# Kernel optimization log

Hardware: AMD Instinct MI355X
Metric: run time of the kernel (lower is better)

Reference implementation:

```python
import jax, jax.numpy as jnp
import numpy as np

D_MODEL = 256
D_STATE = 256          # n_state == embedding_dim in this module
D_INNER = 2 * D_MODEL  # mamba expand=2
DT_RANK = D_MODEL // 16
D_CONV = 4
N_BLOCKS = 2
BATCH, SEQLEN = 2, 512


def setup_inputs() -> dict:
    key = jax.random.key(0)
    ks = jax.random.split(key, 10)

    def rn(k, shape, s=0.02):
        return (jax.random.normal(k, shape) * s).astype(jnp.float32)

    # S4D-real style A init: A_log = log(1..d_state), tiled per channel
    A_log = jnp.tile(
        jnp.log(jnp.arange(1, D_STATE + 1, dtype=jnp.float32))[None, None, :],
        (N_BLOCKS, D_INNER, 1),
    )
    return {
        "x": jax.random.normal(ks[0], (BATCH, SEQLEN, D_MODEL), dtype=jnp.float32),
        "in_proj_w": rn(ks[1], (N_BLOCKS, 2 * D_INNER, D_MODEL)),
        "conv_w": rn(ks[2], (N_BLOCKS, D_INNER, D_CONV), 0.3),
        "conv_b": jnp.zeros((N_BLOCKS, D_INNER), jnp.float32),
        "x_proj_w": rn(ks[3], (N_BLOCKS, DT_RANK + 2 * D_STATE, D_INNER)),
        "dt_proj_w": rn(ks[4], (N_BLOCKS, D_INNER, DT_RANK), 0.1),
        # softplus^{-1}(0.01): dt starts around 0.01 as in mamba init
        "dt_proj_b": jnp.full((N_BLOCKS, D_INNER), float(np.log(np.expm1(0.01))), jnp.float32),
        "A_log": A_log,
        "D": jnp.ones((N_BLOCKS, D_INNER), jnp.float32),
        "out_proj_w": rn(ks[5], (N_BLOCKS, D_MODEL, D_INNER)),
        "ffn_w1": rn(ks[6], (N_BLOCKS, 4 * D_MODEL, D_MODEL)),
        "ffn_b1": jnp.zeros((N_BLOCKS, 4 * D_MODEL), jnp.float32),
        "ffn_w2": rn(ks[7], (N_BLOCKS, D_MODEL, 4 * D_MODEL)),
        "ffn_b2": jnp.zeros((N_BLOCKS, D_MODEL), jnp.float32),
    }


def _mamba(x, in_w, cw, cb, xpw, dtw, dtb, A_log, Dp, ow):
    Bb, Ls, _ = x.shape
    xz = jnp.einsum('bld,ed->ble', x, in_w)            # (B,L,2*d_inner)
    xc, z = jnp.split(xz, 2, axis=-1)
    # causal depthwise conv1d over time (kernel D_CONV, left pad D_CONV-1)
    xp = jnp.pad(xc, ((0, 0), (D_CONV - 1, 0), (0, 0)))
    xconv = sum(xp[:, k:k + Ls, :] * cw[:, k] for k in range(D_CONV)) + cb
    xconv = jax.nn.silu(xconv)                          # (B,L,d_inner)
    x_dbl = jnp.einsum('bld,ed->ble', xconv, xpw)       # (B,L,dt_rank+2*d_state)
    dt = x_dbl[..., :DT_RANK]
    Bm = x_dbl[..., DT_RANK:DT_RANK + D_STATE]
    Cm = x_dbl[..., DT_RANK + D_STATE:]
    dt = jax.nn.softplus(jnp.einsum('blr,dr->bld', dt, dtw) + dtb)  # (B,L,d_inner)
    A = -jnp.exp(A_log)                                 # (d_inner,d_state)

    def step(h, inp):
        dt_t, B_t, C_t, x_t = inp                       # (B,di),(B,ds),(B,ds),(B,di)
        h = jnp.exp(dt_t[..., None] * A) * h + (dt_t * x_t)[..., None] * B_t[:, None, :]
        return h, jnp.einsum('bds,bs->bd', h, C_t)

    h0 = jnp.zeros((Bb, D_INNER, D_STATE), dtype=x.dtype)
    _, ys = jax.lax.scan(
        step, h0,
        (dt.swapaxes(0, 1), Bm.swapaxes(0, 1), Cm.swapaxes(0, 1), xconv.swapaxes(0, 1)),
    )
    y = ys.swapaxes(0, 1) + xconv * Dp
    y = y * jax.nn.silu(z)
    return jnp.einsum('bld,ed->ble', y, ow)


def reference(x, in_proj_w, conv_w, conv_b, x_proj_w, dt_proj_w, dt_proj_b,
              A_log, D, out_proj_w, ffn_w1, ffn_b1, ffn_w2, ffn_b2):
    # VanillaMambaBlock.forward: x = ffn(mamba(x))  (norms/residual unused in source)
    for i in range(N_BLOCKS):
        h = _mamba(x, in_proj_w[i], conv_w[i], conv_b[i], x_proj_w[i],
                   dt_proj_w[i], dt_proj_b[i], A_log[i], D[i], out_proj_w[i])
        h = jax.nn.gelu(jnp.einsum('bld,fd->blf', h, ffn_w1[i]) + ffn_b1[i], approximate=False)
        x = jnp.einsum('blf,ef->ble', h, ffn_w2[i]) + ffn_b2[i]
    return x
```

## Files before the change

kernel.cpp:

```cpp
#include <hip/hip_runtime.h>
#include <math.h>

#define BATCHN 2
#define SEQLEN 512
#define DMODEL 256
#define DSTATE 256
#define DINNER 512
#define DTRANK 16
#define MROWS (BATCHN * SEQLEN)

typedef float f32x4 __attribute__((ext_vector_type(4)));
typedef __bf16 bf16x8 __attribute__((ext_vector_type(8)));

__device__ __forceinline__ float gelu_exact(float v) {
    return 0.5f * v * (1.0f + erff(v * 0.70710678118654752440f));
}
__device__ __forceinline__ float softplus_f(float v) {
    return fmaxf(v, 0.0f) + log1pf(__expf(-fabsf(v)));
}
__device__ __forceinline__ float silu_f(float v) {
    return v / (1.0f + __expf(-v));
}

#define DPP_ADD(X, CTRL)                                                              \
    {                                                                                 \
        int dpp_t_ = __builtin_amdgcn_update_dpp(                                     \
            0, __builtin_bit_cast(int, (X)), (CTRL), 0xf, 0xf, true);                 \
        (X) += __builtin_bit_cast(float, dpp_t_);                                     \
    }
#define DPP_REDUCE32(X)                                                               \
    DPP_ADD(X, 0x111) DPP_ADD(X, 0x112) DPP_ADD(X, 0x114) DPP_ADD(X, 0x118)          \
    DPP_ADD(X, 0x142)

__device__ __forceinline__ void split8(float4 u, float4 v, bf16x8& hi, bf16x8& lo) {
#define SP8(idx, val) { __bf16 h_ = (__bf16)(val); hi[idx] = h_; lo[idx] = (__bf16)((val) - (float)h_); }
    SP8(0, u.x) SP8(1, u.y) SP8(2, u.z) SP8(3, u.w)
    SP8(4, v.x) SP8(5, v.y) SP8(6, v.z) SP8(7, v.w)
#undef SP8
}

template <int NF, int EPI>
__global__ __launch_bounds__(256) void gemm_mfma_kernel(
    const float* __restrict__ A, int lda,
    const float* __restrict__ W,
    const float* __restrict__ bias,
    float* __restrict__ C, int ldc,
    int N, int K)
{
    const int tid = threadIdx.x;
    const int wv = tid >> 6;
    const int lane = tid & 63;
    const int l15 = lane & 15;
    const int kgrp = lane >> 4;
    const int m0 = blockIdx.y * 64 + wv * 16;
    const int n0 = blockIdx.x * (16 * NF);

    const float* ap = A + (size_t)(m0 + l15) * lda + kgrp * 8;
    const float* bp[NF];
#pragma unroll
    for (int nf = 0; nf < NF; ++nf) {
        int col = n0 + nf * 16 + l15;
        if (col >= N) col = N - 1;
        bp[nf] = W + (size_t)col * K + kgrp * 8;
    }

    f32x4 acc[NF];
#pragma unroll
    for (int nf = 0; nf < NF; ++nf) acc[nf] = (f32x4){0.f, 0.f, 0.f, 0.f};

    float4 ar0 = *(const float4*)ap, ar1 = *(const float4*)(ap + 4);
    float4 br0[NF], br1[NF];
#pragma unroll
    for (int nf = 0; nf < NF; ++nf) {
        br0[nf] = *(const float4*)bp[nf];
        br1[nf] = *(const float4*)(bp[nf] + 4);
    }

    for (int k0 = 0; k0 < K; k0 += 32) {
        const int adv = (k0 + 32 < K) ? 32 : 0;
        ap += adv;
        float4 an0 = *(const float4*)ap, an1 = *(const float4*)(ap + 4);
        float4 bn0[NF], bn1[NF];
#pragma unroll
        for (int nf = 0; nf < NF; ++nf) {
            bp[nf] += adv;
            bn0[nf] = *(const float4*)bp[nf];
            bn1[nf] = *(const float4*)(bp[nf] + 4);
        }
        bf16x8 ahi, alo;
        split8(ar0, ar1, ahi, alo);
#pragma unroll
        for (int nf = 0; nf < NF; ++nf) {
            bf16x8 bhi, blo;
            split8(br0[nf], br1[nf], bhi, blo);
            acc[nf] = __builtin_amdgcn_mfma_f32_16x16x32_bf16(ahi, bhi, acc[nf], 0, 0, 0);
            acc[nf] = __builtin_amdgcn_mfma_f32_16x16x32_bf16(ahi, blo, acc[nf], 0, 0, 0);
            acc[nf] = __builtin_amdgcn_mfma_f32_16x16x32_bf16(alo, bhi, acc[nf], 0, 0, 0);
        }
        ar0 = an0; ar1 = an1;
#pragma unroll
        for (int nf = 0; nf < NF; ++nf) { br0[nf] = bn0[nf]; br1[nf] = bn1[nf]; }
    }

#pragma unroll
    for (int nf = 0; nf < NF; ++nf) {
        const int col = n0 + nf * 16 + l15;
        const bool cok = (col < N);
        float bv = 0.f;
        if (EPI >= 1 && cok) bv = bias[col];
#pragma unroll
        for (int j = 0; j < 4; ++j) {
            const int row = m0 + kgrp * 4 + j;
            float v = acc[nf][j];
            if (EPI >= 1) v += bv;
            if (EPI == 2) v = gelu_exact(v);
            if (cok) C[(size_t)row * ldc + col] = v;
        }
    }
}

template <int EPI>
__global__ __launch_bounds__(128) void gemm_kernel(
    const float* __restrict__ A, int lda,
    const float* __restrict__ W,
    const float* __restrict__ bias,
    float* __restrict__ C, int ldc,
    int M, int N, int K)
{
    __shared__ float As[32 * 32];
    __shared__ float Ws[32 * 32];
    const int tid = threadIdx.x;
    const int tx = tid & 15, ty = tid >> 4;
    const int m0 = blockIdx.y * 32, n0 = blockIdx.x * 32;
    const int lrow = tid >> 2;
    const int lk = (tid & 3) << 3;

    float acc[4][2] = {};

    for (int k0 = 0; k0 < K; k0 += 32) {
        const float* arow = A + (size_t)(m0 + lrow) * lda + k0 + lk;
        float4 a0 = *(const float4*)(arow);
        float4 a1 = *(const float4*)(arow + 4);
        int wrow = n0 + lrow;
        if (wrow >= N) wrow = N - 1;
        const float* wp = W + (size_t)wrow * K + k0 + lk;
        float4 w0 = {0,0,0,0}, w1 = {0,0,0,0};
        if (k0 + lk + 3 < K) w0 = *(const float4*)(wp);
        if (k0 + lk + 7 < K) w1 = *(const float4*)(wp + 4);
        __syncthreads();
        As[(lk + 0) * 32 + lrow] = a0.x;
        As[(lk + 1) * 32 + lrow] = a0.y;
        As[(lk + 2) * 32 + lrow] = a0.z;
        As[(lk + 3) * 32 + lrow] = a0.w;
        As[(lk + 4) * 32 + lrow] = a1.x;
        As[(lk + 5) * 32 + lrow] = a1.y;
        As[(lk + 6) * 32 + lrow] = a1.z;
        As[(lk + 7) * 32 + lrow] = a1.w;
        Ws[(lk + 0) * 32 + lrow] = w0.x;
        Ws[(lk + 1) * 32 + lrow] = w0.y;
        Ws[(lk + 2) * 32 + lrow] = w0.z;
        Ws[(lk + 3) * 32 + lrow] = w0.w;
        Ws[(lk + 4) * 32 + lrow] = w1.x;
        Ws[(lk + 5) * 32 + lrow] = w1.y;
        Ws[(lk + 6) * 32 + lrow] = w1.z;
        Ws[(lk + 7) * 32 + lrow] = w1.w;
        __syncthreads();
#pragma unroll
        for (int k = 0; k < 32; ++k) {
            float4 av = *(const float4*)(As + k * 32 + (ty << 2));
            float2 wv = *(const float2*)(Ws + k * 32 + (tx << 1));
            float ar[4] = {av.x, av.y, av.z, av.w};
            float wr[2] = {wv.x, wv.y};
#pragma unroll
            for (int i = 0; i < 4; ++i)
#pragma unroll
                for (int j = 0; j < 2; ++j)
                    acc[i][j] = fmaf(ar[i], wr[j], acc[i][j]);
        }
    }

#pragma unroll
    for (int i = 0; i < 4; ++i) {
        const int row = m0 + (ty << 2) + i;
#pragma unroll
        for (int j = 0; j < 2; ++j) {
            const int col = n0 + (tx << 1) + j;
            if (col < N) {
                float v = acc[i][j];
                if (EPI >= 1) v += bias[col];
                if (EPI == 2) v = gelu_exact(v);
                if (EPI == 3) v = softplus_f(v);
                C[(size_t)row * ldc + col] = v;
            }
        }
    }
}

__global__ __launch_bounds__(256) void conv_silu_kernel(
    const float* __restrict__ xz, const float* __restrict__ cw,
    const float* __restrict__ cb, float* __restrict__ xconv)
{
    int idx = blockIdx.x * blockDim.x + threadIdx.x;
    if (idx >= MROWS * DINNER) return;
    int d = idx & (DINNER - 1);
    int bl = idx >> 9;
    int l = bl & (SEQLEN - 1);
    int b = bl >> 9;
    float s = cb[d];
#pragma unroll
    for (int k = 0; k < 4; ++k) {
        int ls = l + k - 3;
        if (ls >= 0)
            s += xz[((size_t)(b * SEQLEN + ls)) * 1024 + d] * cw[d * 4 + k];
    }
    xconv[idx] = silu_f(s);
}

#define SCAN_STEP_A(DT, XV, ZV, B0, B1, C0, C1)                                      \
    {                                                                                \
        const float rho = __expf(-(DT));                                             \
        const float a0 = __expf(Afirst * (DT));                                      \
        const float val = (DT) * (XV);                                               \
        sumdt += (DT);                                                               \
        const float rho2 = rho * rho, rho4 = rho2 * rho2;                            \
        float a = a0;                                                                \
        h[0] = fmaf(a, h[0], val * (B0).x); float acA = h[0] * (C0).x; a *= rho;     \
        h[1] = fmaf(a, h[1], val * (B0).y); float acB = h[1] * (C0).y; a *= rho;     \
        h[2] = fmaf(a, h[2], val * (B0).z); acA = fmaf(h[2], (C0).z, acA); a *= rho; \
        h[3] = fmaf(a, h[3], val * (B0).w); acB = fmaf(h[3], (C0).w, acB);           \
        a = a0 * rho4;                                                               \
        h[4] = fmaf(a, h[4], val * (B1).x); acA = fmaf(h[4], (C1).x, acA); a *= rho; \
        h[5] = fmaf(a, h[5], val * (B1).y); acB = fmaf(h[5], (C1).y, acB); a *= rho; \
        h[6] = fmaf(a, h[6], val * (B1).z); acA = fmaf(h[6], (C1).z, acA); a *= rho; \
        h[7] = fmaf(a, h[7], val * (B1).w); acB = fmaf(h[7], (C1).w, acB);           \
        float acc = acA + acB;                                                       \
        DPP_REDUCE32(acc)                                                            \
        if (t == 31) y[o1 - 1024] = (acc + (XV) * Dd) * silu_f(ZV);                  \
    }

__global__ __launch_bounds__(256, 6) void scan_passA_kernel(
    const float* __restrict__ dtv, const float* __restrict__ xconv,
    const float* __restrict__ xdbl, const float* __restrict__ xz,
    const float* __restrict__ Dp,
    float* __restrict__ y, float* __restrict__ hend, float* __restrict__ sumdtb,
    int NC, int LC)
{
    const int c = blockIdx.x;
    const int bdo = blockIdx.y;
    const int b = bdo >> 6;
    const int tid = threadIdx.x;
    const int t = tid & 31;
    const int d = ((bdo & 63) << 3) + (tid >> 5);

    const float Afirst = -(float)(8 * t + 1);
    const float Dd = Dp[d];

    float h[8];
#pragma unroll
    for (int k = 0; k < 8; ++k) h[k] = 0.f;
    float sumdt = 0.f;

    const int bl0 = b * SEQLEN + c * LC;
    const float* xB = xdbl + 16;
    const float* xC = xdbl + 272;
    unsigned o1 = (unsigned)(bl0 * 512 + d);
    unsigned o2 = (unsigned)(bl0 * 1024 + 512 + d);
    unsigned o3 = (unsigned)(bl0 * 528 + t * 8);

    float dt0 = dtv[o1], xv0 = xconv[o1], zv0 = xz[o2];
    float4 B00 = *(const float4*)(xB + o3), B01 = *(const float4*)(xB + o3 + 4);
    float4 C00 = *(const float4*)(xC + o3), C01 = *(const float4*)(xC + o3 + 4);
    o1 += 512; o2 += 1024; o3 += 528;

    for (int il = 0; il < LC; il += 2) {
        float dt1 = dtv[o1], xv1 = xconv[o1], zv1 = xz[o2];
        float4 B10 = *(const float4*)(xB + o3), B11 = *(const float4*)(xB + o3 + 4);
        float4 C10 = *(const float4*)(xC + o3), C11 = *(const float4*)(xC + o3 + 4);
        o1 += 512; o2 += 1024; o3 += 528;
        SCAN_STEP_A(dt0, xv0, zv0, B00, B01, C00, C01);
        dt0 = dtv[o1]; xv0 = xconv[o1]; zv0 = xz[o2];
        B00 = *(const float4*)(xB + o3); B01 = *(const float4*)(xB + o3 + 4);
        C00 = *(const float4*)(xC + o3); C01 = *(const float4*)(xC + o3 + 4);
        o1 += 512; o2 += 1024; o3 += 528;
        SCAN_STEP_A(dt1, xv1, zv1, B10, B11, C10, C11);
    }

    const size_t sb = ((size_t)(b * 512 + d) * NC + c) * 256 + t * 8;
    *(float4*)(hend + sb)     = make_float4(h[0], h[1], h[2], h[3]);
    *(float4*)(hend + sb + 4) = make_float4(h[4], h[5], h[6], h[7]);
    if (t == 0) sumdtb[(size_t)(b * 512 + d) * NC + c] = sumdt;
}

__global__ __launch_bounds__(64) void scan_passB_kernel(
    float* __restrict__ hend, const float* __restrict__ sumdtb, int NC)
{
    const int bd = blockIdx.x;
    const int lane = threadIdx.x;
    const float As0 = -(float)(4 * lane + 1);
    const float As1 = As0 - 1.f, As2 = As0 - 2.f, As3 = As0 - 3.f;
    float4 hin = {0.f, 0.f, 0.f, 0.f};
    for (int c = 0; c < NC; ++c) {
        const float sdt = sumdtb[(size_t)bd * NC + c];
        const size_t sidx = ((size_t)bd * NC + c) * DSTATE + (lane << 2);
        float4 he = *(const float4*)(hend + sidx);
        float4 p;
        p.x = __expf(As0 * sdt);
        p.y = __expf(As1 * sdt);
        p.z = __expf(As2 * sdt);
        p.w = __expf(As3 * sdt);
        *(float4*)(hend + sidx) = hin;
        float4 nh;
        nh.x = fmaf(p.x, hin.x, he.x);
        nh.y = fmaf(p.y, hin.y, he.y);
        nh.z = fmaf(p.z, hin.z, he.z);
        nh.w = fmaf(p.w, hin.w, he.w);
        hin = nh;
    }
}

#define SCAN_STEP_C(DT, ZV, C0, C1)                                                  \
    {                                                                                \
        const float rho = __expf(-(DT));                                             \
        const float a0 = __expf(Afirst * (DT));                                      \
        const float rho2 = rho * rho, rho4 = rho2 * rho2;                            \
        float a = a0;                                                                \
        carry[0] *= a; float acA = carry[0] * (C0).x; a *= rho;                      \
        carry[1] *= a; float acB = carry[1] * (C0).y; a *= rho;                      \
        carry[2] *= a; acA = fmaf(carry[2], (C0).z, acA); a *= rho;                  \
        carry[3] *= a; acB = fmaf(carry[3], (C0).w, acB);                            \
        a = a0 * rho4;                                                               \
        carry[4] *= a; acA = fmaf(carry[4], (C1).x, acA); a *= rho;                  \
        carry[5] *= a; acB = fmaf(carry[5], (C1).y, acB); a *= rho;                  \
        carry[6] *= a; acA = fmaf(carry[6], (C1).z, acA); a *= rho;                  \
        carry[7] *= a; acB = fmaf(carry[7], (C1).w, acB);                            \
        float acc = acA + acB;                                                       \
        DPP_REDUCE32(acc)                                                            \
        if (t == 31) y[o1 - 1024] += acc * silu_f(ZV);                               \
    }

__global__ __launch_bounds__(256, 8) void scan_passC_kernel(
    const float* __restrict__ dtv, const float* __restrict__ xdbl,
    const float* __restrict__ xz, const float* __restrict__ hend,
    float* __restrict__ y, int NC, int LC)
{
    const int c = blockIdx.x + 1;
    const int bdo = blockIdx.y;
    const int b = bdo >> 6;
    const int tid = threadIdx.x;
    const int t = tid & 31;
    const int d = ((bdo & 63) << 3) + (tid >> 5);

    const float Afirst = -(float)(8 * t + 1);

    float carry[8];
    const size_t sb = ((size_t)(b * 512 + d) * NC + c) * 256 + t * 8;
    {
        float4 c0 = *(const float4*)(hend + sb);
        float4 c1 = *(const float4*)(hend + sb + 4);
        carry[0] = c0.x; carry[1] = c0.y; carry[2] = c0.z; carry[3] = c0.w;
        carry[4] = c1.x; carry[5] = c1.y; carry[6] = c1.z; carry[7] = c1.w;
    }

    const int bl0 = b * SEQLEN + c * LC;
    const float* xC = xdbl + 272;
    unsigned o1 = (unsigned)(bl0 * 512 + d);
    unsigned o2 = (unsigned)(bl0 * 1024 + 512 + d);
    unsigned o3 = (unsigned)(bl0 * 528 + t * 8);

    float dt0 = dtv[o1], zv0 = xz[o2];
    float4 C00 = *(const float4*)(xC + o3), C01 = *(const float4*)(xC + o3 + 4);
    o1 += 512; o2 += 1024; o3 += 528;

    for (int il = 0; il < LC; il += 2) {
        float dt1 = dtv[o1], zv1 = xz[o2];
        float4 C10 = *(const float4*)(xC + o3), C11 = *(const float4*)(xC + o3 + 4);
        o1 += 512; o2 += 1024; o3 += 528;
        SCAN_STEP_C(dt0, zv0, C00, C01);
        dt0 = dtv[o1]; zv0 = xz[o2];
        C00 = *(const float4*)(xC + o3); C01 = *(const float4*)(xC + o3 + 4);
        o1 += 512; o2 += 1024; o3 += 528;
        SCAN_STEP_C(dt1, zv1, C10, C11);
    }
}

extern "C" void kernel_launch(void* const* d_in, const int* in_sizes, int n_in,
                              void* d_out, int out_size, void* d_ws, size_t ws_size,
                              hipStream_t stream) {
    const float* x     = (const float*)d_in[0];
    const float* in_w  = (const float*)d_in[1];
    const float* cw    = (const float*)d_in[2];
    const float* cb    = (const float*)d_in[3];
    const float* xpw   = (const float*)d_in[4];
    const float* dtw   = (const float*)d_in[5];
    const float* dtb   = (const float*)d_in[6];
    const float* Dp    = (const float*)d_in[8];
    const float* ow    = (const float*)d_in[9];
    const float* w1    = (const float*)d_in[10];
    const float* b1    = (const float*)d_in[11];
    const float* w2    = (const float*)d_in[12];
    const float* b2    = (const float*)d_in[13];

    float* ws = (float*)d_ws;
    float* xzb   = ws;
    float* xcv   = xzb + 1024 * 1024;
    float* xdbl  = xcv + 1024 * 512;
    float* dtv   = xdbl + 1024 * 528;
    float* yb    = dtv + 1024 * 512;
    float* hendb = yb + 1024 * 512;
    const size_t baseFloats = 1024*1024 + 1024*512 + 1024*528 + 1024*512 + 1024*512;
    int NC = 16;
    while (NC > 1 && (baseFloats + (size_t)NC * 1024 * 256 + (size_t)NC * 1024) * 4ull > ws_size) NC >>= 1;
    const int LC = SEQLEN / NC;
    float* sumdtb = hendb + (size_t)NC * 1024 * 256;

    float* mo    = xcv;
    float* h1b   = xzb;
    float* x1    = xdbl;

    const float* xin = x;
    for (int i = 0; i < 2; ++i) {
        const float* inw_i = in_w + (size_t)i * 1024 * 256;
        const float* cw_i  = cw  + (size_t)i * 512 * 4;
        const float* cb_i  = cb  + (size_t)i * 512;
        const float* xpw_i = xpw + (size_t)i * 528 * 512;
        const float* dtw_i = dtw + (size_t)i * 512 * 16;
        const float* dtb_i = dtb + (size_t)i * 512;
        const float* Dp_i  = Dp  + (size_t)i * 512;
        const float* ow_i  = ow  + (size_t)i * 256 * 512;
        const float* w1_i  = w1  + (size_t)i * 1024 * 256;
        const float* b1_i  = b1  + (size_t)i * 1024;
        const float* w2_i  = w2  + (size_t)i * 256 * 1024;
        const float* b2_i  = b2  + (size_t)i * 256;

        gemm_mfma_kernel<2, 0><<<dim3(32, 16), 256, 0, stream>>>(xin, DMODEL, inw_i, nullptr, xzb, 1024, 1024, 256);
        conv_silu_kernel<<<(MROWS * DINNER + 255) / 256, 256, 0, stream>>>(xzb, cw_i, cb_i, xcv);
        gemm_mfma_kernel<2, 0><<<dim3(17, 16), 256, 0, stream>>>(xcv, DINNER, xpw_i, nullptr, xdbl, 528, 528, 512);
        gemm_kernel<3><<<dim3(16, 32), 128, 0, stream>>>(xdbl, 528, dtw_i, dtb_i, dtv, 512, MROWS, 512, 16);
        scan_passA_kernel<<<dim3(NC, 128), 256, 0, stream>>>(dtv, xcv, xdbl, xzb, Dp_i, yb, hendb, sumdtb, NC, LC);
        if (NC > 1) {
            scan_passB_kernel<<<MROWS, 64, 0, stream>>>(hendb, sumdtb, NC);
            scan_passC_kernel<<<dim3(NC - 1, 128), 256, 0, stream>>>(dtv, xdbl, xzb, hendb, yb, NC, LC);
        }
        gemm_mfma_kernel<1, 0><<<dim3(16, 16), 256, 0, stream>>>(yb, DINNER, ow_i, nullptr, mo, 256, 256, 512);
        gemm_mfma_kernel<2, 2><<<dim3(32, 16), 256, 0, stream>>>(mo, 256, w1_i, b1_i, h1b, 1024, 1024, 256);
        float* outp = (i == 1) ? (float*)d_out : x1;
        gemm_mfma_kernel<1, 1><<<dim3(16, 16), 256, 0, stream>>>(h1b, 1024, w2_i, b2_i, outp, 256, 256, 1024);
        xin = x1;
    }
}
```

Measured before the change: 356.9 us.

## Stage scan B/C and per-step scalars through double-buffered swizzled LDS

Scan passes A and C now load B/C rows and the dt/x/z scalars cooperatively into double-buffered shared memory, four timesteps at a time, instead of each wave loading them redundantly from global memory. A XOR swizzle on LDS addresses is meant to avoid bank conflicts on the float4 reads. The goal is to cut duplicated global and L2 traffic across the 8 channel-waves in a block. In exchange it adds a block-wide barrier every four steps, extra LDS use, and lowers pass A's occupancy hint from 6 to 5. It also assumes LC is a multiple of 4.

Result: faster. 335.2 us (-6.1%).

```diff
diff --git a/kernel.cpp b/kernel.cpp
--- a/kernel.cpp
+++ b/kernel.cpp
@@ -20,6 +20,9 @@
 }
 __device__ __forceinline__ float silu_f(float v) {
     return v / (1.0f + __expf(-v));
+}
+__device__ __forceinline__ unsigned swzw(unsigned w) {
+    return w ^ (((w >> 5) & 7u) << 2);
 }
 
 #define DPP_ADD(X, CTRL)                                                              \
@@ -216,73 +219,107 @@
     xconv[idx] = silu_f(s);
 }
 
-#define SCAN_STEP_A(DT, XV, ZV, B0, B1, C0, C1)                                      \
-    {                                                                                \
-        const float rho = __expf(-(DT));                                             \
-        const float a0 = __expf(Afirst * (DT));                                      \
-        const float val = (DT) * (XV);                                               \
-        sumdt += (DT);                                                               \
-        const float rho2 = rho * rho, rho4 = rho2 * rho2;                            \
-        float a = a0;                                                                \
-        h[0] = fmaf(a, h[0], val * (B0).x); float acA = h[0] * (C0).x; a *= rho;     \
-        h[1] = fmaf(a, h[1], val * (B0).y); float acB = h[1] * (C0).y; a *= rho;     \
-        h[2] = fmaf(a, h[2], val * (B0).z); acA = fmaf(h[2], (C0).z, acA); a *= rho; \
-        h[3] = fmaf(a, h[3], val * (B0).w); acB = fmaf(h[3], (C0).w, acB);           \
-        a = a0 * rho4;                                                               \
-        h[4] = fmaf(a, h[4], val * (B1).x); acA = fmaf(h[4], (C1).x, acA); a *= rho; \
-        h[5] = fmaf(a, h[5], val * (B1).y); acB = fmaf(h[5], (C1).y, acB); a *= rho; \
-        h[6] = fmaf(a, h[6], val * (B1).z); acA = fmaf(h[6], (C1).z, acA); a *= rho; \
-        h[7] = fmaf(a, h[7], val * (B1).w); acB = fmaf(h[7], (C1).w, acB);           \
-        float acc = acA + acB;                                                       \
-        DPP_REDUCE32(acc)                                                            \
-        if (t == 31) y[o1 - 1024] = (acc + (XV) * Dd) * silu_f(ZV);                  \
-    }
-
-__global__ __launch_bounds__(256, 6) void scan_passA_kernel(
+__global__ __launch_bounds__(256, 5) void scan_passA_kernel(
     const float* __restrict__ dtv, const float* __restrict__ xconv,
     const float* __restrict__ xdbl, const float* __restrict__ xz,
     const float* __restrict__ Dp,
     float* __restrict__ y, float* __restrict__ hend, float* __restrict__ sumdtb,
     int NC, int LC)
 {
+    __shared__ float bc[2][4][512];
+    __shared__ float ssc[2][3][4][8];
+
     const int c = blockIdx.x;
     const int bdo = blockIdx.y;
     const int b = bdo >> 6;
+    const int d0 = (bdo & 63) << 3;
     const int tid = threadIdx.x;
     const int t = tid & 31;
-    const int d = ((bdo & 63) << 3) + (tid >> 5);
+    const int hw = tid >> 5;
+    const int d = d0 + hw;
 
     const float Afirst = -(float)(8 * t + 1);
     const float Dd = Dp[d];
+    const int bl0 = b * SEQLEN + c * LC;
+
+    const int si = tid >> 7;
+    const int sF = tid & 127;
+    const unsigned wdst = swzw(4u * sF);
+    const int sarr = tid >> 5;
+    const int sri = (tid & 31) >> 3, sdd = tid & 7;
+    const float* pBC0 = xdbl + (size_t)(bl0 + si) * 528 + 16 + 4 * sF;
+    const float* pBC1 = pBC0 + 2 * 528;
+    const float* sbase;
+    unsigned sstep;
+    if (sarr == 0)      { sbase = dtv   + (size_t)(bl0 + sri) * 512 + d0 + sdd;        sstep = 2048; }
+    else if (sarr == 1) { sbase = xconv + (size_t)(bl0 + sri) * 512 + d0 + sdd;        sstep = 2048; }
+    else                { sbase = xz    + (size_t)(bl0 + sri) * 1024 + 512 + d0 + sdd; sstep = 4096; }
+
+    const unsigned sw = ((unsigned)(t >> 2)) << 2;
+    const unsigned wb0 = (8u * t) ^ sw;
+    const unsigned wb1 = (8u * t + 4u) ^ sw;
+    const unsigned wc0 = (256u + 8u * t) ^ sw;
+    const unsigned wc1 = (256u + 8u * t + 4u) ^ sw;
 
     float h[8];
 #pragma unroll
     for (int k = 0; k < 8; ++k) h[k] = 0.f;
     float sumdt = 0.f;
 
-    const int bl0 = b * SEQLEN + c * LC;
-    const float* xB = xdbl + 16;
-    const float* xC = xdbl + 272;
-    unsigned o1 = (unsigned)(bl0 * 512 + d);
-    unsigned o2 = (unsigned)(bl0 * 1024 + 512 + d);
-    unsigned o3 = (unsigned)(bl0 * 528 + t * 8);
-
-    float dt0 = dtv[o1], xv0 = xconv[o1], zv0 = xz[o2];
-    float4 B00 = *(const float4*)(xB + o3), B01 = *(const float4*)(xB + o3 + 4);
-    float4 C00 = *(const float4*)(xC + o3), C01 = *(const float4*)(xC + o3 + 4);
-    o1 += 512; o2 += 1024; o3 += 528;
-
-    for (int il = 0; il < LC; il += 2) {
-        float dt1 = dtv[o1], xv1 = xconv[o1], zv1 = xz[o2];
-        float4 B10 = *(const float4*)(xB + o3), B11 = *(const float4*)(xB + o3 + 4);
-        float4 C10 = *(const float4*)(xC + o3), C11 = *(const float4*)(xC + o3 + 4);
-        o1 += 512; o2 += 1024; o3 += 528;
-        SCAN_STEP_A(dt0, xv0, zv0, B00, B01, C00, C01);
-        dt0 = dtv[o1]; xv0 = xconv[o1]; zv0 = xz[o2];
-        B00 = *(const float4*)(xB + o3); B01 = *(const float4*)(xB + o3 + 4);
-        C00 = *(const float4*)(xC + o3); C01 = *(const float4*)(xC + o3 + 4);
-        o1 += 512; o2 += 1024; o3 += 528;
-        SCAN_STEP_A(dt1, xv1, zv1, B10, B11, C10, C11);
+    float4 rBC0 = *(const float4*)pBC0;
+    float4 rBC1 = *(const float4*)pBC1;
+    float rS = (sarr < 3) ? *sbase : 0.f;
+    *(float4*)&bc[0][si][wdst] = rBC0;
+    *(float4*)&bc[0][2 + si][wdst] = rBC1;
+    if (sarr < 3) ssc[0][sarr][sri][sdd] = rS;
+    __syncthreads();
+
+    const int G = LC >> 2;
+    unsigned ybase = (unsigned)(bl0 * 512 + d);
+    for (int g = 0; g < G; ++g) {
+        const int buf = g & 1;
+        if (g + 1 < G) {
+            rBC0 = *(const float4*)(pBC0 + (unsigned)(g + 1) * 2112u);
+            rBC1 = *(const float4*)(pBC1 + (unsigned)(g + 1) * 2112u);
+            if (sarr < 3) rS = sbase[(unsigned)(g + 1) * sstep];
+        }
+#pragma unroll
+        for (int i = 0; i < 4; ++i) {
+            const float dt = ssc[buf][0][i][hw];
+            const float xv = ssc[buf][1][i][hw];
+            const float zv = ssc[buf][2][i][hw];
+            const float* brow = &bc[buf][i][0];
+            float4 B0 = *(const float4*)(brow + wb0);
+            float4 B1 = *(const float4*)(brow + wb1);
+            float4 C0 = *(const float4*)(brow + wc0);
+            float4 C1 = *(const float4*)(brow + wc1);
+            const float rho = __expf(-dt);
+            const float a0 = __expf(Afirst * dt);
+            const float val = dt * xv;
+            sumdt += dt;
+            const float rho2 = rho * rho, rho4 = rho2 * rho2;
+            float a = a0;
+            h[0] = fmaf(a, h[0], val * B0.x); float acA = h[0] * C0.x; a *= rho;
+            h[1] = fmaf(a, h[1], val * B0.y); float acB = h[1] * C0.y; a *= rho;
+            h[2] = fmaf(a, h[2], val * B0.z); acA = fmaf(h[2], C0.z, acA); a *= rho;
+            h[3] = fmaf(a, h[3], val * B0.w); acB = fmaf(h[3], C0.w, acB);
+            a = a0 * rho4;
+            h[4] = fmaf(a, h[4], val * B1.x); acA = fmaf(h[4], C1.x, acA); a *= rho;
+            h[5] = fmaf(a, h[5], val * B1.y); acB = fmaf(h[5], C1.y, acB); a *= rho;
+            h[6] = fmaf(a, h[6], val * B1.z); acA = fmaf(h[6], C1.z, acA); a *= rho;
+            h[7] = fmaf(a, h[7], val * B1.w); acB = fmaf(h[7], C1.w, acB);
+            float acc = acA + acB;
+            DPP_REDUCE32(acc)
+            if (t == 31) y[ybase + i * 512] = (acc + xv * Dd) * silu_f(zv);
+        }
+        ybase += 2048;
+        if (g + 1 < G) {
+            const int nbuf = buf ^ 1;
+            *(float4*)&bc[nbuf][si][wdst] = rBC0;
+            *(float4*)&bc[nbuf][2 + si][wdst] = rBC1;
+            if (sarr < 3) ssc[nbuf][sarr][sri][sdd] = rS;
+        }
+        __syncthreads();
     }
 
     const size_t sb = ((size_t)(b * 512 + d) * NC + c) * 256 + t * 8;
@@ -318,39 +355,40 @@
     }
 }
 
-#define SCAN_STEP_C(DT, ZV, C0, C1)                                                  \
-    {                                                                                \
-        const float rho = __expf(-(DT));                                             \
-        const float a0 = __expf(Afirst * (DT));                                      \
-        const float rho2 = rho * rho, rho4 = rho2 * rho2;                            \
-        float a = a0;                                                                \
-        carry[0] *= a; float acA = carry[0] * (C0).x; a *= rho;                      \
-        carry[1] *= a; float acB = carry[1] * (C0).y; a *= rho;                      \
-        carry[2] *= a; acA = fmaf(carry[2], (C0).z, acA); a *= rho;                  \
-        carry[3] *= a; acB = fmaf(carry[3], (C0).w, acB);                            \
-        a = a0 * rho4;                                                               \
-        carry[4] *= a; acA = fmaf(carry[4], (C1).x, acA); a *= rho;                  \
-        carry[5] *= a; acB = fmaf(carry[5], (C1).y, acB); a *= rho;                  \
-        carry[6] *= a; acA = fmaf(carry[6], (C1).z, acA); a *= rho;                  \
-        carry[7] *= a; acB = fmaf(carry[7], (C1).w, acB);                            \
-        float acc = acA + acB;                                                       \
-        DPP_REDUCE32(acc)                                                            \
-        if (t == 31) y[o1 - 1024] += acc * silu_f(ZV);                               \
-    }
-
 __global__ __launch_bounds__(256, 8) void scan_passC_kernel(
     const float* __restrict__ dtv, const float* __restrict__ xdbl,
     const float* __restrict__ xz, const float* __restrict__ hend,
     float* __restrict__ y, int NC, int LC)
 {
+    __shared__ float cc[2][4][256];
+    __shared__ float ssd[2][2][4][8];
+
     const int c = blockIdx.x + 1;
     const int bdo = blockIdx.y;
     const int b = bdo >> 6;
+    const int d0 = (bdo & 63) << 3;
     const int tid = threadIdx.x;
     const int t = tid & 31;
-    const int d = ((bdo & 63) << 3) + (tid >> 5);
+    const int hw = tid >> 5;
+    const int d = d0 + hw;
 
     const float Afirst = -(float)(8 * t + 1);
+    const int bl0 = b * SEQLEN + c * LC;
+
+    const int si = tid >> 6;
+    const int sF = tid & 63;
+    const unsigned wdst = swzw(4u * sF);
+    const int sarr = tid >> 5;
+    const int sri = (tid & 31) >> 3, sdd = tid & 7;
+    const float* pC = xdbl + (size_t)(bl0 + si) * 528 + 272 + 4 * sF;
+    const float* sbase;
+    unsigned sstep;
+    if (sarr == 0) { sbase = dtv + (size_t)(bl0 + sri) * 512 + d0 + sdd;        sstep = 2048; }
+    else           { sbase = xz  + (size_t)(bl0 + sri) * 1024 + 512 + d0 + sdd; sstep = 4096; }
+
+    const unsigned sw = ((unsigned)(t >> 2)) << 2;
+    const unsigned wc0 = (8u * t) ^ sw;
+    const unsigned wc1 = (8u * t + 4u) ^ sw;
 
     float carry[8];
     const size_t sb = ((size_t)(b * 512 + d) * NC + c) * 256 + t * 8;
@@ -361,25 +399,51 @@
         carry[4] = c1.x; carry[5] = c1.y; carry[6] = c1.z; carry[7] = c1.w;
     }
 
-    const int bl0 = b * SEQLEN + c * LC;
-    const float* xC = xdbl + 272;
-    unsigned o1 = (unsigned)(bl0 * 512 + d);
-    unsigned o2 = (unsigned)(bl0 * 1024 + 512 + d);
-    unsigned o3 = (unsigned)(bl0 * 528 + t * 8);
-
-    float dt0 = dtv[o1], zv0 = xz[o2];
-    float4 C00 = *(const float4*)(xC + o3), C01 = *(const float4*)(xC + o3 + 4);
-    o1 += 512; o2 += 1024; o3 += 528;
-
-    for (int il = 0; il < LC; il += 2) {
-        float dt1 = dtv[o1], zv1 = xz[o2];
-        float4 C10 = *(const float4*)(xC + o3), C11 = *(const float4*)(xC + o3 + 4);
-        o1 += 512; o2 += 1024; o3 += 528;
-        SCAN_STEP_C(dt0, zv0, C00, C01);
-        dt0 = dtv[o1]; zv0 = xz[o2];
-        C00 = *(const float4*)(xC + o3); C01 = *(const float4*)(xC + o3 + 4);
-        o1 += 512; o2 += 1024; o3 += 528;
-        SCAN_STEP_C(dt1, zv1, C10, C11);
+    float4 rC = *(const float4*)pC;
+    float rS = (sarr < 2) ? *sbase : 0.f;
+    *(float4*)&cc[0][si][wdst] = rC;
+    if (sarr < 2) ssd[0][sarr][sri][sdd] = rS;
+    __syncthreads();
+
+    const int G = LC >> 2;
+    unsigned ybase = (unsigned)(bl0 * 512 + d);
+    for (int g = 0; g < G; ++g) {
+        const int buf = g & 1;
+        if (g + 1 < G) {
+            rC = *(const float4*)(pC + (unsigned)(g + 1) * 2112u);
+            if (sarr < 2) rS = sbase[(unsigned)(g + 1) * sstep];
+        }
+#pragma unroll
+        for (int i = 0; i < 4; ++i) {
+            const float dt = ssd[buf][0][i][hw];
+            const float zv = ssd[buf][1][i][hw];
+            const float* crow = &cc[buf][i][0];
+            float4 C0 = *(const float4*)(crow + wc0);
+            float4 C1 = *(const float4*)(crow + wc1);
+            const float rho = __expf(-dt);
+            const float a0 = __expf(Afirst * dt);
+            const float rho2 = rho * rho, rho4 = rho2 * rho2;
+            float a = a0;
+            carry[0] *= a; float acA = carry[0] * C0.x; a *= rho;
+            carry[1] *= a; float acB = carry[1] * C0.y; a *= rho;
+            carry[2] *= a; acA = fmaf(carry[2], C0.z, acA); a *= rho;
+            carry[3] *= a; acB = fmaf(carry[3], C0.w, acB);
+            a = a0 * rho4;
+            carry[4] *= a; acA = fmaf(carry[4], C1.x, acA); a *= rho;
+            carry[5] *= a; acB = fmaf(carry[5], C1.y, acB); a *= rho;
+            carry[6] *= a; acA = fmaf(carry[6], C1.z, acA); a *= rho;
+            carry[7] *= a; acB = fmaf(carry[7], C1.w, acB);
+            float acc = acA + acB;
+            DPP_REDUCE32(acc)
+            if (t == 31) y[ybase + i * 512] += acc * silu_f(zv);
+        }
+        ybase += 2048;
+        if (g + 1 < G) {
+            const int nbuf = buf ^ 1;
+            *(float4*)&cc[nbuf][si][wdst] = rC;
+            if (sarr < 2) ssd[nbuf][sarr][sri][sdd] = rS;
+        }
+        __syncthreads();
     }
 }
 
```
